# Kernel optimization log

Measured on AMD Instinct MI355X. Metric: run time of the kernel, lower is better.

## Reference

```python
import jax, jax.numpy as jnp
import numpy as np

EPS = 1e-6


def _rms_norm(x, w):
    # RMSNorm over last dim in fp32, like Qwen3RMSNorm
    x32 = x.astype(jnp.float32)
    var = jnp.mean(x32 * x32, axis=-1, keepdims=True)
    return (x32 * jax.lax.rsqrt(var + EPS)).astype(x.dtype) * w


def _rotate_half(x):
    h = x.shape[-1] // 2
    return jnp.concatenate([-x[..., h:], x[..., :h]], axis=-1)


def setup_inputs() -> dict:
    key = jax.random.key(0)
    ks = jax.random.split(key, 8)
    B, S, HID = 1, 8192, 1024
    H, HKV, D = 16, 8, 128
    n_seg = 8
    hidden_states = jax.random.normal(ks[0], (B, S, HID), dtype=jnp.float32)
    cu_seqlens = jnp.arange(n_seg + 1, dtype=jnp.int32) * (S // n_seg)
    # multimodal RoPE tables: two position streams, each [B, S, D]
    inv_freq = 1.0 / (1e6 ** (jnp.arange(0, D, 2, dtype=jnp.float32) / D))
    pos = jnp.arange(S, dtype=jnp.float32)
    ang0 = pos[:, None] * inv_freq[None, :]            # [S, D/2]
    ang1 = (pos[:, None] * 0.5) * inv_freq[None, :]    # second stream
    def tab(a):
        return jnp.concatenate([a, a], axis=-1)[None]   # [1, S, D]
    cos = jnp.stack([tab(jnp.cos(ang0)), tab(jnp.cos(ang1))], axis=0)  # [2,1,S,D]
    sin = jnp.stack([tab(jnp.sin(ang0)), tab(jnp.sin(ang1))], axis=0)
    sd = 0.02
    Wq = jax.random.normal(ks[1], (H * D, HID), dtype=jnp.float32) * sd
    Wk = jax.random.normal(ks[2], (HKV * D, HID), dtype=jnp.float32) * sd
    Wv = jax.random.normal(ks[3], (HKV * D, HID), dtype=jnp.float32) * sd
    Wo = jax.random.normal(ks[4], (HID, H * D), dtype=jnp.float32) * sd
    q_norm_w = 1.0 + jax.random.normal(ks[5], (D,), dtype=jnp.float32) * sd
    k_norm_w = 1.0 + jax.random.normal(ks[6], (D,), dtype=jnp.float32) * sd
    return {"hidden_states": hidden_states, "cu_seqlens": cu_seqlens,
            "cos": cos, "sin": sin, "Wq": Wq, "Wk": Wk, "Wv": Wv, "Wo": Wo,
            "q_norm_w": q_norm_w, "k_norm_w": k_norm_w}


def reference(hidden_states, cu_seqlens, cos, sin, Wq, Wk, Wv, Wo, q_norm_w, k_norm_w):
    B, S, _ = hidden_states.shape
    D = q_norm_w.shape[0]
    H = Wq.shape[0] // D
    HKV = Wk.shape[0] // D
    groups = H // HKV
    n_seg = cu_seqlens.shape[0] - 1   # equal-length segments (static)
    L = S // n_seg
    scaling = D ** -0.5

    # projections -> [B, H(kv), S, D]
    q = (hidden_states @ Wq.T).reshape(B, S, H, D).transpose(0, 2, 1, 3)
    k = (hidden_states @ Wk.T).reshape(B, S, HKV, D).transpose(0, 2, 1, 3)
    v = (hidden_states @ Wv.T).reshape(B, S, HKV, D).transpose(0, 2, 1, 3)

    q = _rms_norm(q, q_norm_w)
    k = _rms_norm(k, k_norm_w)

    # multimodal RoPE: interleave the two streams across the two half-dims
    half = D // 2
    cos_e = jnp.concatenate([cos[0, ..., :half], cos[1, ..., half:]], axis=-1)[:, None]  # [B,1,S,D]
    sin_e = jnp.concatenate([sin[0, ..., :half], sin[1, ..., half:]], axis=-1)[:, None]
    q = q * cos_e + _rotate_half(q) * sin_e
    k = k * cos_e + _rotate_half(k) * sin_e

    # GQA: repeat kv heads
    k = jnp.repeat(k, groups, axis=1)
    v = jnp.repeat(v, groups, axis=1)

    # block-diagonal attention over cu_seqlens segments (equal-length -> reshape)
    qb = q.reshape(B, H, n_seg, L, D)
    kb = k.reshape(B, H, n_seg, L, D)
    vb = v.reshape(B, H, n_seg, L, D)
    scores = jnp.einsum('bhnld,bhnmd->bhnlm', qb, kb) * scaling
    probs = jax.nn.softmax(scores, axis=-1)
    ob = jnp.einsum('bhnlm,bhnmd->bhnld', probs, vb)
    out = ob.reshape(B, H, S, D).transpose(0, 2, 1, 3).reshape(B, S, H * D)
    return out @ Wo.T
```

## Files before the change

### kernel.cpp

```cpp
#include <hip/hip_runtime.h>

#define S_LEN 8192
#define HID   1024
#define NH    16
#define NKV   8
#define HD    128
#define LSEG  1024

typedef float  f4  __attribute__((ext_vector_type(4)));
typedef _Float16 h4 __attribute__((ext_vector_type(4)));
typedef _Float16 h8 __attribute__((ext_vector_type(8)));

__device__ __forceinline__ void gl_lds16(const void* g, void* l) {
  __builtin_amdgcn_global_load_lds((const __attribute__((address_space(1))) void*)g,
                                   (__attribute__((address_space(3))) void*)l, 16, 0, 0);
}

__device__ __forceinline__ h8 ld8u(const _Float16* p) {
  h4 a = *(const h4*)p;
  h4 b = *(const h4*)(p + 4);
  return __builtin_shufflevector(a, b, 0, 1, 2, 3, 4, 5, 6, 7);
}

template <int CTRL>
__device__ __forceinline__ float dppf(float v) {
  return __builtin_bit_cast(float,
      __builtin_amdgcn_mov_dpp(__builtin_bit_cast(int, v), CTRL, 0xF, 0xF, true));
}
__device__ __forceinline__ float red16_max(float x) {
  x = fmaxf(x, dppf<0xB1>(x));
  x = fmaxf(x, dppf<0x4E>(x));
  x = fmaxf(x, dppf<0x141>(x));
  x = fmaxf(x, dppf<0x140>(x));
  return x;
}
__device__ __forceinline__ float red16_sum(float x) {
  x += dppf<0xB1>(x);
  x += dppf<0x4E>(x);
  x += dppf<0x141>(x);
  x += dppf<0x140>(x);
  return x;
}

__global__ void convert_kernel(const float* __restrict__ hid, const float* __restrict__ wq,
                               const float* __restrict__ wk, const float* __restrict__ wv,
                               const float* __restrict__ wo,
                               _Float16* __restrict__ hid16, _Float16* __restrict__ wqkv,
                               _Float16* __restrict__ wo16) {
  const int total4 = 3670016;
  for (int i = blockIdx.x * blockDim.x + threadIdx.x; i < total4; i += gridDim.x * blockDim.x) {
    int i4 = i * 4;
    const float* src; _Float16* dst;
    if      (i4 <  8388608) { src = hid + i4;              dst = hid16 + i4; }
    else if (i4 < 10485760) { src = wq + (i4 -  8388608);  dst = wqkv + (i4 - 8388608); }
    else if (i4 < 11534336) { src = wk + (i4 - 10485760);  dst = wqkv + 2097152 + (i4 - 10485760); }
    else if (i4 < 12582912) { src = wv + (i4 - 11534336);  dst = wqkv + 3145728 + (i4 - 11534336); }
    else                    { src = wo + (i4 - 12582912);  dst = wo16 + (i4 - 12582912); }
    f4 x = *(const f4*)src;
    h4 y; y[0]=(_Float16)x[0]; y[1]=(_Float16)x[1]; y[2]=(_Float16)x[2]; y[3]=(_Float16)x[3];
    *(h4*)dst = y;
  }
}

template <int FUSED>
__global__ __launch_bounds__(256, 3)
void gemm_kernel(const _Float16* __restrict__ A, const _Float16* __restrict__ B,
                 float* __restrict__ Cout, int K, int N,
                 const float* __restrict__ cosp, const float* __restrict__ sinp,
                 const float* __restrict__ qnw, const float* __restrict__ knw,
                 _Float16* __restrict__ q16, _Float16* __restrict__ k16,
                 _Float16* __restrict__ v16T) {
  __shared__ __align__(16) char smem[32768];

  constexpr int GX  = FUSED ? 32 : 8;
  constexpr int NWG = FUSED ? 2048 : 512;
  const int lin = blockIdx.y * GX + blockIdx.x;
  const int swz = (lin & 7) * (NWG >> 3) + (lin >> 3);
  const int bx = swz & (GX - 1), by = swz / GX;

  const int tid = threadIdx.x, w = tid >> 6, ln = tid & 63;
  const int l15 = ln & 15, l4 = ln >> 4;
  const int m0 = by * 128, n0 = bx * 128;
  const int sg_row = ln >> 2, sg_cho = (ln & 3) * 8;

  f4 acc[2][8] = {};

  for (int k0 = 0; k0 < K; k0 += 64) {
    __syncthreads();
#pragma unroll
    for (int r = 0; r < 2; r++) {
      int ch = r * 4 + w;
#pragma unroll
      for (int u = 0; u < 2; u++) {
        gl_lds16(A + (size_t)(m0 + ch * 16 + sg_row) * K + k0 + u * 32 + sg_cho,
                 smem + u * 8192 + ch * 1024);
        gl_lds16(B + (size_t)(n0 + ch * 16 + sg_row) * K + k0 + u * 32 + sg_cho,
                 smem + 16384 + u * 8192 + ch * 1024);
      }
    }
    __syncthreads();
#pragma unroll
    for (int u = 0; u < 2; u++) {
      const _Float16* As = (const _Float16*)(smem + u * 8192);
      const _Float16* Bs = (const _Float16*)(smem + 16384 + u * 8192);
      h8 af[2], bf[8];
#pragma unroll
      for (int mt = 0; mt < 2; mt++) af[mt] = *(const h8*)(As + (w * 32 + mt * 16 + l15) * 32 + l4 * 8);
#pragma unroll
      for (int nt = 0; nt < 8; nt++) bf[nt] = *(const h8*)(Bs + (nt * 16 + l15) * 32 + l4 * 8);
#pragma unroll
      for (int mt = 0; mt < 2; mt++)
#pragma unroll
        for (int nt = 0; nt < 8; nt++)
          acc[mt][nt] = __builtin_amdgcn_mfma_f32_16x16x32_f16(af[mt], bf[nt], acc[mt][nt], 0, 0, 0);
    }
  }

  if (!FUSED) {
#pragma unroll
    for (int mt = 0; mt < 2; mt++)
#pragma unroll
      for (int rg = 0; rg < 4; rg++) {
        int row = m0 + w * 32 + mt * 16 + l4 * 4 + rg;
#pragma unroll
        for (int nt = 0; nt < 8; nt++)
          Cout[(size_t)row * N + n0 + nt * 16 + l15] = acc[mt][nt][rg];
      }
    return;
  } else {
    const int head = bx;
    if (head < 24) {
      const float* nw = (head < 16) ? qnw : knw;
      const float hs = (head < 16) ? 0.12751734f : 1.0f;
      _Float16* base = (head < 16) ? q16 + (size_t)head * S_LEN * HD
                                   : k16 + (size_t)(head - 16) * S_LEN * HD;
      float nwv[8];
#pragma unroll
      for (int nt = 0; nt < 8; nt++) nwv[nt] = nw[nt * 16 + l15];
#pragma unroll
      for (int mt = 0; mt < 2; mt++)
#pragma unroll
        for (int rg = 0; rg < 4; rg++) {
          const int row = m0 + w * 32 + mt * 16 + l4 * 4 + rg;
          float ss = 0.f;
#pragma unroll
          for (int nt = 0; nt < 8; nt++) ss += acc[mt][nt][rg] * acc[mt][nt][rg];
          ss = red16_sum(ss);
          const float sc = rsqrtf(ss * 0.0078125f + 1e-6f);
#pragma unroll
          for (int nt = 0; nt < 8; nt++) {
            const int c = nt * 16 + l15;
            const int str = (nt >= 4) ? 1048576 : 0;
            float x  = acc[mt][nt][rg] * sc * nwv[nt];
            float xp = acc[mt][nt ^ 4][rg] * sc * nwv[nt ^ 4];
            float ce = cosp[str + row * HD + c];
            float se = sinp[str + row * HD + c];
            float rot = (nt >= 4) ? xp : -xp;
            base[(size_t)row * HD + c] = (_Float16)((x * ce + rot * se) * hs);
          }
        }
    } else {
      _Float16* vb = v16T + (size_t)(head - 24) * S_LEN * HD;
#pragma unroll
      for (int mt = 0; mt < 2; mt++)
#pragma unroll
        for (int nt = 0; nt < 8; nt++) {
          h4 hv;
#pragma unroll
          for (int rg = 0; rg < 4; rg++) hv[rg] = (_Float16)acc[mt][nt][rg];
          *(h4*)&vb[(size_t)(nt * 16 + l15) * S_LEN + m0 + w * 32 + mt * 16 + l4 * 4] = hv;
        }
    }
  }
}

__global__ __launch_bounds__(256, 2)
void attn_kernel(const _Float16* __restrict__ q16, const _Float16* __restrict__ k16,
                 const _Float16* __restrict__ vT, _Float16* __restrict__ ao16) {
  const int bid = blockIdx.x;
  const int xcd = bid & 7, slot = bid >> 3;
  const int grp = xcd * 8 + (slot >> 4);
  const int mem = slot & 15;
  const int g = grp >> 3, hkv = grp & 7;
  const int tq = mem & 7, h = hkv * 2 + (mem >> 3);

  const int tid = threadIdx.x, w = tid >> 6, ln = tid & 63;
  const int l15 = ln & 15, l4 = ln >> 4;

  __shared__ _Float16 Qs[128 * 132];
  __shared__ _Float16 KP[128 * 68];
  __shared__ _Float16 Vt[128 * 68];

  const _Float16* qsrc = q16 + ((size_t)h * S_LEN + g * LSEG + tq * 128) * HD;
#pragma unroll
  for (int i = 0; i < 8; i++) {
    int c = tid + 256 * i, row = c >> 4, o = c & 15;
    uint4 v = *(const uint4*)(qsrc + row * HD + o * 8);
    *(uint2*)&Qs[row * 132 + o * 8]     = make_uint2(v.x, v.y);
    *(uint2*)&Qs[row * 132 + o * 8 + 4] = make_uint2(v.z, v.w);
  }

  f4 O[2][8] = {};
  float mr[2][4], lr[2][4];
#pragma unroll
  for (int mt = 0; mt < 2; mt++)
#pragma unroll
    for (int rg = 0; rg < 4; rg++) { mr[mt][rg] = -1e30f; lr[mt][rg] = 0.f; }

  const size_t kbase = ((size_t)hkv * S_LEN + g * LSEG) * HD;
  const size_t vbase = (size_t)hkv * S_LEN * HD + (size_t)g * LSEG;

  const int krow = tid >> 4, ko = tid & 15;
  const int vd   = tid >> 3, vo = tid & 7;

  uint4 kr[4], vr[4];
#pragma unroll
  for (int i = 0; i < 4; i++) {
    kr[i] = *(const uint4*)(k16 + kbase + (size_t)(krow + 16 * i) * HD + ko * 8);
    vr[i] = *(const uint4*)(vT + vbase + (size_t)(vd + 32 * i) * S_LEN + vo * 8);
  }
#pragma unroll
  for (int i = 0; i < 4; i++) {
    int row = krow + 16 * i;
    *(uint2*)&KP[row * 132 + ko * 8]     = make_uint2(kr[i].x, kr[i].y);
    *(uint2*)&KP[row * 132 + ko * 8 + 4] = make_uint2(kr[i].z, kr[i].w);
    int d = vd + 32 * i;
    *(uint2*)&Vt[d * 68 + vo * 8]     = make_uint2(vr[i].x, vr[i].y);
    *(uint2*)&Vt[d * 68 + vo * 8 + 4] = make_uint2(vr[i].z, vr[i].w);
  }

  for (int j = 0; j < 16; j++) {
    __syncthreads();

    const int jn = (j + 1) & 15;
#pragma unroll
    for (int i = 0; i < 4; i++) {
      kr[i] = *(const uint4*)(k16 + kbase + (size_t)(jn * 64 + krow + 16 * i) * HD + ko * 8);
      vr[i] = *(const uint4*)(vT + vbase + (size_t)(vd + 32 * i) * S_LEN + jn * 64 + vo * 8);
    }

    f4 s[2][4] = {};
    __builtin_amdgcn_s_setprio(1);
#pragma unroll
    for (int kk = 0; kk < 4; kk++) {
      h8 a0 = ld8u(Qs + (w * 32 + l15) * 132 + kk * 32 + l4 * 8);
      h8 a1 = ld8u(Qs + (w * 32 + 16 + l15) * 132 + kk * 32 + l4 * 8);
#pragma unroll
      for (int nt = 0; nt < 4; nt++) {
        h8 b = ld8u(KP + (nt * 16 + l15) * 132 + kk * 32 + l4 * 8);
        s[0][nt] = __builtin_amdgcn_mfma_f32_16x16x32_f16(a0, b, s[0][nt], 0, 0, 0);
        s[1][nt] = __builtin_amdgcn_mfma_f32_16x16x32_f16(a1, b, s[1][nt], 0, 0, 0);
      }
    }
    __builtin_amdgcn_s_setprio(0);

    float mx[2][4];
    bool nd = false;
#pragma unroll
    for (int mt = 0; mt < 2; mt++)
#pragma unroll
      for (int rg = 0; rg < 4; rg++) {
        float m = fmaxf(fmaxf(s[mt][0][rg], s[mt][1][rg]), fmaxf(s[mt][2][rg], s[mt][3][rg]));
        m = red16_max(m);
        mx[mt][rg] = m;
        nd = nd || (m > mr[mt][rg] + 8.f);
      }
    const bool needr = __any((int)nd) != 0;
    float al[2][4];
    if (needr) {
#pragma unroll
      for (int mt = 0; mt < 2; mt++)
#pragma unroll
        for (int rg = 0; rg < 4; rg++) {
          float mnew = fmaxf(mr[mt][rg], mx[mt][rg]);
          al[mt][rg] = exp2f(mr[mt][rg] - mnew);
          mr[mt][rg] = mnew;
        }
    }
#pragma unroll
    for (int mt = 0; mt < 2; mt++)
#pragma unroll
      for (int rg = 0; rg < 4; rg++) {
        float rs = 0.f;
#pragma unroll
        for (int nt = 0; nt < 4; nt++) {
          float p = exp2f(s[mt][nt][rg] - mr[mt][rg]);
          s[mt][nt][rg] = p;
          rs += p;
        }
        rs = red16_sum(rs);
        if (needr) lr[mt][rg] = lr[mt][rg] * al[mt][rg] + rs;
        else       lr[mt][rg] += rs;
      }

    __syncthreads();
#pragma unroll
    for (int mt = 0; mt < 2; mt++)
#pragma unroll
      for (int nt = 0; nt < 4; nt++)
#pragma unroll
        for (int rg = 0; rg < 4; rg++)
          KP[(w * 32 + mt * 16 + l4 * 4 + rg) * 68 + nt * 16 + l15] = (_Float16)s[mt][nt][rg];
    if (needr) {
#pragma unroll
      for (int mt = 0; mt < 2; mt++)
#pragma unroll
        for (int d8 = 0; d8 < 8; d8++)
#pragma unroll
          for (int rg = 0; rg < 4; rg++) O[mt][d8][rg] *= al[mt][rg];
    }

    __builtin_amdgcn_s_setprio(1);
#pragma unroll
    for (int kk = 0; kk < 2; kk++) {
      h8 a0 = ld8u(KP + (w * 32 + l15) * 68 + kk * 32 + l4 * 8);
      h8 a1 = ld8u(KP + (w * 32 + 16 + l15) * 68 + kk * 32 + l4 * 8);
#pragma unroll
      for (int d8 = 0; d8 < 8; d8++) {
        h8 b = ld8u(Vt + (d8 * 16 + l15) * 68 + kk * 32 + l4 * 8);
        O[0][d8] = __builtin_amdgcn_mfma_f32_16x16x32_f16(a0, b, O[0][d8], 0, 0, 0);
        O[1][d8] = __builtin_amdgcn_mfma_f32_16x16x32_f16(a1, b, O[1][d8], 0, 0, 0);
      }
    }
    __builtin_amdgcn_s_setprio(0);

    __syncthreads();
#pragma unroll
    for (int i = 0; i < 4; i++) {
      int row = krow + 16 * i;
      *(uint2*)&KP[row * 132 + ko * 8]     = make_uint2(kr[i].x, kr[i].y);
      *(uint2*)&KP[row * 132 + ko * 8 + 4] = make_uint2(kr[i].z, kr[i].w);
      int d = vd + 32 * i;
      *(uint2*)&Vt[d * 68 + vo * 8]     = make_uint2(vr[i].x, vr[i].y);
      *(uint2*)&Vt[d * 68 + vo * 8 + 4] = make_uint2(vr[i].z, vr[i].w);
    }
  }

  const size_t obase = (size_t)(g * LSEG + tq * 128);
#pragma unroll
  for (int mt = 0; mt < 2; mt++)
#pragma unroll
    for (int rg = 0; rg < 4; rg++) {
      float inv = 1.f / lr[mt][rg];
#pragma unroll
      for (int d8 = 0; d8 < 8; d8++)
        ao16[(obase + w * 32 + mt * 16 + l4 * 4 + rg) * 2048 + h * HD + d8 * 16 + l15] =
            (_Float16)(O[mt][d8][rg] * inv);
    }
}

extern "C" void kernel_launch(void* const* d_in, const int* in_sizes, int n_in,
                              void* d_out, int out_size, void* d_ws, size_t ws_size,
                              hipStream_t stream) {
  const float* hid  = (const float*)d_in[0];
  const float* cosp = (const float*)d_in[2];
  const float* sinp = (const float*)d_in[3];
  const float* wq   = (const float*)d_in[4];
  const float* wk   = (const float*)d_in[5];
  const float* wv   = (const float*)d_in[6];
  const float* wo   = (const float*)d_in[7];
  const float* qnw  = (const float*)d_in[8];
  const float* knw  = (const float*)d_in[9];
  float* out = (float*)d_out;

  _Float16* hid16 = (_Float16*)d_ws;
  _Float16* wqkv  = hid16 + 8388608;
  _Float16* wo16  = wqkv + 4194304;
  _Float16* q16   = wo16 + 2097152;
  _Float16* k16   = q16 + 16777216;
  _Float16* v16T  = k16 + 8388608;
  _Float16* ao16  = v16T + 8388608;

  convert_kernel<<<dim3(1024), dim3(256), 0, stream>>>(hid, wq, wk, wv, wo, hid16, wqkv, wo16);
  gemm_kernel<1><<<dim3(32, 64), dim3(256), 0, stream>>>(hid16, wqkv, nullptr, 1024, 4096,
                                                         cosp, sinp, qnw, knw, q16, k16, v16T);
  attn_kernel<<<dim3(1024), dim3(256), 0, stream>>>(q16, k16, v16T, ao16);
  gemm_kernel<0><<<dim3(8, 64), dim3(256), 0, stream>>>(ao16, wo16, out, 2048, 1024,
                                                        nullptr, nullptr, nullptr, nullptr,
                                                        nullptr, nullptr, nullptr);
}
```

Measured before the change: 401.1 us.

## Split attention block across 8 waves with 16 query rows each

The attention kernel moves from 256 to 512 threads per block, with each of 8 waves owning 16 query rows instead of 32. Per-thread accumulators, softmax state and K/V staging registers are halved, and launch bounds rise to (512,4) to allow more resident waves for latency hiding. In exchange, each wave now reuses every K/V fragment read from LDS for only one MFMA instead of two, doubling LDS read traffic per FLOP, and the extra waves add barrier cost.

```diff
diff --git a/kernel.cpp b/kernel.cpp
--- a/kernel.cpp
+++ b/kernel.cpp
@@ -174,7 +174,7 @@
   }
 }
 
-__global__ __launch_bounds__(256, 2)
+__global__ __launch_bounds__(512, 4)
 void attn_kernel(const _Float16* __restrict__ q16, const _Float16* __restrict__ k16,
                  const _Float16* __restrict__ vT, _Float16* __restrict__ ao16) {
   const int bid = blockIdx.x;
@@ -193,19 +193,17 @@
 
   const _Float16* qsrc = q16 + ((size_t)h * S_LEN + g * LSEG + tq * 128) * HD;
 #pragma unroll
-  for (int i = 0; i < 8; i++) {
-    int c = tid + 256 * i, row = c >> 4, o = c & 15;
+  for (int i = 0; i < 4; i++) {
+    int c = tid + 512 * i, row = c >> 4, o = c & 15;
     uint4 v = *(const uint4*)(qsrc + row * HD + o * 8);
     *(uint2*)&Qs[row * 132 + o * 8]     = make_uint2(v.x, v.y);
     *(uint2*)&Qs[row * 132 + o * 8 + 4] = make_uint2(v.z, v.w);
   }
 
-  f4 O[2][8] = {};
-  float mr[2][4], lr[2][4];
-#pragma unroll
-  for (int mt = 0; mt < 2; mt++)
-#pragma unroll
-    for (int rg = 0; rg < 4; rg++) { mr[mt][rg] = -1e30f; lr[mt][rg] = 0.f; }
+  f4 O[8] = {};
+  float mr[4], lr[4];
+#pragma unroll
+  for (int rg = 0; rg < 4; rg++) { mr[rg] = -1e30f; lr[rg] = 0.f; }
 
   const size_t kbase = ((size_t)hkv * S_LEN + g * LSEG) * HD;
   const size_t vbase = (size_t)hkv * S_LEN * HD + (size_t)g * LSEG;
@@ -213,18 +211,18 @@
   const int krow = tid >> 4, ko = tid & 15;
   const int vd   = tid >> 3, vo = tid & 7;
 
-  uint4 kr[4], vr[4];
-#pragma unroll
-  for (int i = 0; i < 4; i++) {
-    kr[i] = *(const uint4*)(k16 + kbase + (size_t)(krow + 16 * i) * HD + ko * 8);
-    vr[i] = *(const uint4*)(vT + vbase + (size_t)(vd + 32 * i) * S_LEN + vo * 8);
-  }
-#pragma unroll
-  for (int i = 0; i < 4; i++) {
-    int row = krow + 16 * i;
+  uint4 kr[2], vr[2];
+#pragma unroll
+  for (int i = 0; i < 2; i++) {
+    kr[i] = *(const uint4*)(k16 + kbase + (size_t)(krow + 32 * i) * HD + ko * 8);
+    vr[i] = *(const uint4*)(vT + vbase + (size_t)(vd + 64 * i) * S_LEN + vo * 8);
+  }
+#pragma unroll
+  for (int i = 0; i < 2; i++) {
+    int row = krow + 32 * i;
     *(uint2*)&KP[row * 132 + ko * 8]     = make_uint2(kr[i].x, kr[i].y);
     *(uint2*)&KP[row * 132 + ko * 8 + 4] = make_uint2(kr[i].z, kr[i].w);
-    int d = vd + 32 * i;
+    int d = vd + 64 * i;
     *(uint2*)&Vt[d * 68 + vo * 8]     = make_uint2(vr[i].x, vr[i].y);
     *(uint2*)&Vt[d * 68 + vo * 8 + 4] = make_uint2(vr[i].z, vr[i].w);
   }
@@ -234,103 +232,89 @@
 
     const int jn = (j + 1) & 15;
 #pragma unroll
-    for (int i = 0; i < 4; i++) {
-      kr[i] = *(const uint4*)(k16 + kbase + (size_t)(jn * 64 + krow + 16 * i) * HD + ko * 8);
-      vr[i] = *(const uint4*)(vT + vbase + (size_t)(vd + 32 * i) * S_LEN + jn * 64 + vo * 8);
-    }
-
-    f4 s[2][4] = {};
+    for (int i = 0; i < 2; i++) {
+      kr[i] = *(const uint4*)(k16 + kbase + (size_t)(jn * 64 + krow + 32 * i) * HD + ko * 8);
+      vr[i] = *(const uint4*)(vT + vbase + (size_t)(vd + 64 * i) * S_LEN + jn * 64 + vo * 8);
+    }
+
+    f4 s[4] = {};
     __builtin_amdgcn_s_setprio(1);
 #pragma unroll
     for (int kk = 0; kk < 4; kk++) {
-      h8 a0 = ld8u(Qs + (w * 32 + l15) * 132 + kk * 32 + l4 * 8);
-      h8 a1 = ld8u(Qs + (w * 32 + 16 + l15) * 132 + kk * 32 + l4 * 8);
+      h8 a0 = ld8u(Qs + (w * 16 + l15) * 132 + kk * 32 + l4 * 8);
 #pragma unroll
       for (int nt = 0; nt < 4; nt++) {
         h8 b = ld8u(KP + (nt * 16 + l15) * 132 + kk * 32 + l4 * 8);
-        s[0][nt] = __builtin_amdgcn_mfma_f32_16x16x32_f16(a0, b, s[0][nt], 0, 0, 0);
-        s[1][nt] = __builtin_amdgcn_mfma_f32_16x16x32_f16(a1, b, s[1][nt], 0, 0, 0);
+        s[nt] = __builtin_amdgcn_mfma_f32_16x16x32_f16(a0, b, s[nt], 0, 0, 0);
       }
     }
     __builtin_amdgcn_s_setprio(0);
 
-    float mx[2][4];
+    float mx[4];
     bool nd = false;
 #pragma unroll
-    for (int mt = 0; mt < 2; mt++)
+    for (int rg = 0; rg < 4; rg++) {
+      float m = fmaxf(fmaxf(s[0][rg], s[1][rg]), fmaxf(s[2][rg], s[3][rg]));
+      m = red16_max(m);
+      mx[rg] = m;
+      nd = nd || (m > mr[rg] + 8.f);
+    }
+    const bool needr = __any((int)nd) != 0;
+    float al[4];
+    if (needr) {
 #pragma unroll
       for (int rg = 0; rg < 4; rg++) {
-        float m = fmaxf(fmaxf(s[mt][0][rg], s[mt][1][rg]), fmaxf(s[mt][2][rg], s[mt][3][rg]));
-        m = red16_max(m);
-        mx[mt][rg] = m;
-        nd = nd || (m > mr[mt][rg] + 8.f);
-      }
-    const bool needr = __any((int)nd) != 0;
-    float al[2][4];
+        float mnew = fmaxf(mr[rg], mx[rg]);
+        al[rg] = exp2f(mr[rg] - mnew);
+        mr[rg] = mnew;
+      }
+    }
+#pragma unroll
+    for (int rg = 0; rg < 4; rg++) {
+      float rs = 0.f;
+#pragma unroll
+      for (int nt = 0; nt < 4; nt++) {
+        float p = exp2f(s[nt][rg] - mr[rg]);
+        s[nt][rg] = p;
+        rs += p;
+      }
+      rs = red16_sum(rs);
+      if (needr) lr[rg] = lr[rg] * al[rg] + rs;
+      else       lr[rg] += rs;
+    }
+
+    __syncthreads();
+#pragma unroll
+    for (int nt = 0; nt < 4; nt++)
+#pragma unroll
+      for (int rg = 0; rg < 4; rg++)
+        KP[(w * 16 + l4 * 4 + rg) * 68 + nt * 16 + l15] = (_Float16)s[nt][rg];
     if (needr) {
 #pragma unroll
-      for (int mt = 0; mt < 2; mt++)
-#pragma unroll
-        for (int rg = 0; rg < 4; rg++) {
-          float mnew = fmaxf(mr[mt][rg], mx[mt][rg]);
-          al[mt][rg] = exp2f(mr[mt][rg] - mnew);
-          mr[mt][rg] = mnew;
-        }
-    }
-#pragma unroll
-    for (int mt = 0; mt < 2; mt++)
-#pragma unroll
-      for (int rg = 0; rg < 4; rg++) {
-        float rs = 0.f;
-#pragma unroll
-        for (int nt = 0; nt < 4; nt++) {
-          float p = exp2f(s[mt][nt][rg] - mr[mt][rg]);
-          s[mt][nt][rg] = p;
-          rs += p;
-        }
-        rs = red16_sum(rs);
-        if (needr) lr[mt][rg] = lr[mt][rg] * al[mt][rg] + rs;
-        else       lr[mt][rg] += rs;
-      }
-
-    __syncthreads();
-#pragma unroll
-    for (int mt = 0; mt < 2; mt++)
-#pragma unroll
-      for (int nt = 0; nt < 4; nt++)
-#pragma unroll
-        for (int rg = 0; rg < 4; rg++)
-          KP[(w * 32 + mt * 16 + l4 * 4 + rg) * 68 + nt * 16 + l15] = (_Float16)s[mt][nt][rg];
-    if (needr) {
-#pragma unroll
-      for (int mt = 0; mt < 2; mt++)
-#pragma unroll
-        for (int d8 = 0; d8 < 8; d8++)
-#pragma unroll
-          for (int rg = 0; rg < 4; rg++) O[mt][d8][rg] *= al[mt][rg];
+      for (int d8 = 0; d8 < 8; d8++)
+#pragma unroll
+        for (int rg = 0; rg < 4; rg++) O[d8][rg] *= al[rg];
     }
 
     __builtin_amdgcn_s_setprio(1);
 #pragma unroll
     for (int kk = 0; kk < 2; kk++) {
-      h8 a0 = ld8u(KP + (w * 32 + l15) * 68 + kk * 32 + l4 * 8);
-      h8 a1 = ld8u(KP + (w * 32 + 16 + l15) * 68 + kk * 32 + l4 * 8);
+      h8 a0 = ld8u(KP + (w * 16 + l15) * 68 + kk * 32 + l4 * 8);
 #pragma unroll
       for (int d8 = 0; d8 < 8; d8++) {
         h8 b = ld8u(Vt + (d8 * 16 + l15) * 68 + kk * 32 + l4 * 8);
-        O[0][d8] = __builtin_amdgcn_mfma_f32_16x16x32_f16(a0, b, O[0][d8], 0, 0, 0);
-        O[1][d8] = __builtin_amdgcn_mfma_f32_16x16x32_f16(a1, b, O[1][d8], 0, 0, 0);
+        O[d8] = __builtin_amdgcn_mfma_f32_16x16x32_f16(a0, b, O[d8], 0, 0, 0);
       }
     }
     __builtin_amdgcn_s_setprio(0);
 
     __syncthreads();
 #pragma unroll
-    for (int i = 0; i < 4; i++) {
-      int row = krow + 16 * i;
+    for (int i = 0; i < 2; i++) {
+      int row = krow + 32 * i;
       *(uint2*)&KP[row * 132 + ko * 8]     = make_uint2(kr[i].x, kr[i].y);
       *(uint2*)&KP[row * 132 + ko * 8 + 4] = make_uint2(kr[i].z, kr[i].w);
-      int d = vd + 32 * i;
+      int d = vd + 64 * i;
       *(uint2*)&Vt[d * 68 + vo * 8]     = make_uint2(vr[i].x, vr[i].y);
       *(uint2*)&Vt[d * 68 + vo * 8 + 4] = make_uint2(vr[i].z, vr[i].w);
     }
@@ -338,15 +322,13 @@
 
   const size_t obase = (size_t)(g * LSEG + tq * 128);
 #pragma unroll
-  for (int mt = 0; mt < 2; mt++)
-#pragma unroll
-    for (int rg = 0; rg < 4; rg++) {
-      float inv = 1.f / lr[mt][rg];
-#pragma unroll
-      for (int d8 = 0; d8 < 8; d8++)
-        ao16[(obase + w * 32 + mt * 16 + l4 * 4 + rg) * 2048 + h * HD + d8 * 16 + l15] =
-            (_Float16)(O[mt][d8][rg] * inv);
-    }
+  for (int rg = 0; rg < 4; rg++) {
+    float inv = 1.f / lr[rg];
+#pragma unroll
+    for (int d8 = 0; d8 < 8; d8++)
+      ao16[(obase + w * 16 + l4 * 4 + rg) * 2048 + h * HD + d8 * 16 + l15] =
+          (_Float16)(O[d8][rg] * inv);
+  }
 }
 
 extern "C" void kernel_launch(void* const* d_in, const int* in_sizes, int n_in,
@@ -374,7 +356,7 @@
   convert_kernel<<<dim3(1024), dim3(256), 0, stream>>>(hid, wq, wk, wv, wo, hid16, wqkv, wo16);
   gemm_kernel<1><<<dim3(32, 64), dim3(256), 0, stream>>>(hid16, wqkv, nullptr, 1024, 4096,
                                                          cosp, sinp, qnw, knw, q16, k16, v16T);
-  attn_kernel<<<dim3(1024), dim3(256), 0, stream>>>(q16, k16, v16T, ao16);
+  attn_kernel<<<dim3(1024), dim3(512), 0, stream>>>(q16, k16, v16T, ao16);
   gemm_kernel<0><<<dim3(8, 64), dim3(256), 0, stream>>>(ao16, wo16, out, 2048, 1024,
                                                         nullptr, nullptr, nullptr, nullptr,
                                                         nullptr, nullptr, nullptr);
```

Result: slower. 410.2 us (+2.3%).

## Fold softmax row-sum into PV MFMA via ones column; defer max reduction

Applied to the files above, without the earlier changes.

Appends a ones row to the V tile so the P·V MFMA also produces each row's softmax denominator, removing the per-tile exp-sum and cross-lane reductions. The rescale check now compares raw scores against the threshold per lane, so the DPP max reduction runs only when some lane needs a rescale. This adds two extra MFMAs per k-step and more accumulator registers, and the row sum now comes from fp16-rounded probabilities.

```diff
diff --git a/kernel.cpp b/kernel.cpp
--- a/kernel.cpp
+++ b/kernel.cpp
@@ -40,6 +40,10 @@
   x += dppf<0x141>(x);
   x += dppf<0x140>(x);
   return x;
+}
+__device__ __forceinline__ float bcast16(float v) {
+  return __builtin_bit_cast(float,
+      __builtin_amdgcn_ds_swizzle(__builtin_bit_cast(int, v), 0x0010));
 }
 
 __global__ void convert_kernel(const float* __restrict__ hid, const float* __restrict__ wq,
@@ -189,7 +193,7 @@
 
   __shared__ _Float16 Qs[128 * 132];
   __shared__ _Float16 KP[128 * 68];
-  __shared__ _Float16 Vt[128 * 68];
+  __shared__ _Float16 Vt[144 * 68];
 
   const _Float16* qsrc = q16 + ((size_t)h * S_LEN + g * LSEG + tq * 128) * HD;
 #pragma unroll
@@ -199,13 +203,18 @@
     *(uint2*)&Qs[row * 132 + o * 8]     = make_uint2(v.x, v.y);
     *(uint2*)&Qs[row * 132 + o * 8 + 4] = make_uint2(v.z, v.w);
   }
-
-  f4 O[2][8] = {};
-  float mr[2][4], lr[2][4];
+  if (tid < 68) {
+    Vt[128 * 68 + tid] = (_Float16)1.0f;
+#pragma unroll
+    for (int r = 129; r < 144; r++) Vt[r * 68 + tid] = (_Float16)0.0f;
+  }
+
+  f4 O[2][9] = {};
+  float mr[2][4];
 #pragma unroll
   for (int mt = 0; mt < 2; mt++)
 #pragma unroll
-    for (int rg = 0; rg < 4; rg++) { mr[mt][rg] = -1e30f; lr[mt][rg] = 0.f; }
+    for (int rg = 0; rg < 4; rg++) mr[mt][rg] = -1e30f;
 
   const size_t kbase = ((size_t)hkv * S_LEN + g * LSEG) * HD;
   const size_t vbase = (size_t)hkv * S_LEN * HD + (size_t)g * LSEG;
@@ -254,16 +263,14 @@
     }
     __builtin_amdgcn_s_setprio(0);
 
-    float mx[2][4];
     bool nd = false;
 #pragma unroll
     for (int mt = 0; mt < 2; mt++)
 #pragma unroll
       for (int rg = 0; rg < 4; rg++) {
-        float m = fmaxf(fmaxf(s[mt][0][rg], s[mt][1][rg]), fmaxf(s[mt][2][rg], s[mt][3][rg]));
-        m = red16_max(m);
-        mx[mt][rg] = m;
-        nd = nd || (m > mr[mt][rg] + 8.f);
+        float thr = mr[mt][rg] + 8.f;
+        nd = nd || (s[mt][0][rg] > thr) || (s[mt][1][rg] > thr) ||
+                   (s[mt][2][rg] > thr) || (s[mt][3][rg] > thr);
       }
     const bool needr = __any((int)nd) != 0;
     float al[2][4];
@@ -272,7 +279,9 @@
       for (int mt = 0; mt < 2; mt++)
 #pragma unroll
         for (int rg = 0; rg < 4; rg++) {
-          float mnew = fmaxf(mr[mt][rg], mx[mt][rg]);
+          float m = fmaxf(fmaxf(s[mt][0][rg], s[mt][1][rg]), fmaxf(s[mt][2][rg], s[mt][3][rg]));
+          m = red16_max(m);
+          float mnew = fmaxf(mr[mt][rg], m);
           al[mt][rg] = exp2f(mr[mt][rg] - mnew);
           mr[mt][rg] = mnew;
         }
@@ -280,18 +289,10 @@
 #pragma unroll
     for (int mt = 0; mt < 2; mt++)
 #pragma unroll
-      for (int rg = 0; rg < 4; rg++) {
-        float rs = 0.f;
-#pragma unroll
-        for (int nt = 0; nt < 4; nt++) {
-          float p = exp2f(s[mt][nt][rg] - mr[mt][rg]);
-          s[mt][nt][rg] = p;
-          rs += p;
-        }
-        rs = red16_sum(rs);
-        if (needr) lr[mt][rg] = lr[mt][rg] * al[mt][rg] + rs;
-        else       lr[mt][rg] += rs;
-      }
+      for (int rg = 0; rg < 4; rg++)
+#pragma unroll
+        for (int nt = 0; nt < 4; nt++)
+          s[mt][nt][rg] = exp2f(s[mt][nt][rg] - mr[mt][rg]);
 
     __syncthreads();
 #pragma unroll
@@ -305,7 +306,7 @@
 #pragma unroll
       for (int mt = 0; mt < 2; mt++)
 #pragma unroll
-        for (int d8 = 0; d8 < 8; d8++)
+        for (int d8 = 0; d8 < 9; d8++)
 #pragma unroll
           for (int rg = 0; rg < 4; rg++) O[mt][d8][rg] *= al[mt][rg];
     }
@@ -316,7 +317,7 @@
       h8 a0 = ld8u(KP + (w * 32 + l15) * 68 + kk * 32 + l4 * 8);
       h8 a1 = ld8u(KP + (w * 32 + 16 + l15) * 68 + kk * 32 + l4 * 8);
 #pragma unroll
-      for (int d8 = 0; d8 < 8; d8++) {
+      for (int d8 = 0; d8 < 9; d8++) {
         h8 b = ld8u(Vt + (d8 * 16 + l15) * 68 + kk * 32 + l4 * 8);
         O[0][d8] = __builtin_amdgcn_mfma_f32_16x16x32_f16(a0, b, O[0][d8], 0, 0, 0);
         O[1][d8] = __builtin_amdgcn_mfma_f32_16x16x32_f16(a1, b, O[1][d8], 0, 0, 0);
@@ -341,7 +342,7 @@
   for (int mt = 0; mt < 2; mt++)
 #pragma unroll
     for (int rg = 0; rg < 4; rg++) {
-      float inv = 1.f / lr[mt][rg];
+      float inv = 1.f / bcast16(O[mt][8][rg]);
 #pragma unroll
       for (int d8 = 0; d8 < 8; d8++)
         ao16[(obase + w * 32 + mt * 16 + l4 * 4 + rg) * 2048 + h * HD + d8 * 16 + l15] =
```

New measurement: 389.6 us. -2.9%, faster.
